# Kernel tuning notes

Hardware: AMD Instinct MI355X
Metric: run time of the kernel (lower is better)

Reference implementation:

```python
import jax, jax.numpy as jnp
import numpy as np

N_NODES = 100000
N_EDGES = 1600000
D = 64          # embedding_dim (in_feats == out_feats)
H = 1           # num_heads
NEG_SLOPE = 0.2


def setup_inputs() -> dict:
    key = jax.random.key(0)
    k = jax.random.split(key, 7)
    feat = jax.random.normal(k[0], (N_NODES, D), dtype=jnp.float32)
    W = jax.random.normal(k[1], (D, H * D), dtype=jnp.float32) * (1.0 / np.sqrt(D))
    attn_l = jax.random.normal(k[2], (1, H, D), dtype=jnp.float32) * (1.0 / np.sqrt(D))
    attn_r = jax.random.normal(k[3], (1, H, D), dtype=jnp.float32) * (1.0 / np.sqrt(D))
    bias = jnp.zeros((H * D,), dtype=jnp.float32)
    src = jax.random.randint(k[4], (N_EDGES,), 0, N_NODES, dtype=jnp.int32)
    dst = jax.random.randint(k[5], (N_EDGES,), 0, N_NODES, dtype=jnp.int32)
    return {"feat": feat, "W": W, "attn_l": attn_l, "attn_r": attn_r,
            "bias": bias, "src": src, "dst": dst}


def reference(feat, W, attn_l, attn_r, bias, src, dst):
    # fc (no bias), view to [N, H, D_out]
    ft = (feat @ W).reshape(-1, H, D)                       # [N, H, D]
    # per-node attention halves
    el = jnp.sum(ft * attn_l, axis=-1, keepdims=True)       # [N, H, 1]
    er = jnp.sum(ft * attn_r, axis=-1, keepdims=True)       # [N, H, 1]
    # edge score: u_add_v then leaky_relu
    e = el[src] + er[dst]                                    # [E, H, 1]
    e = jnp.where(e > 0, e, NEG_SLOPE * e)
    # edge softmax over incoming edges of each destination node
    emax = jax.ops.segment_max(e, dst, num_segments=N_NODES)  # [N, H, 1]
    e_exp = jnp.exp(e - emax[dst])
    denom = jax.ops.segment_sum(e_exp, dst, num_segments=N_NODES)  # [N, H, 1]
    a = e_exp / denom[dst]                                   # [E, H, 1]
    # u_mul_e + sum aggregation to destination
    m = ft[src] * a                                          # [E, H, D]
    rst = jax.ops.segment_sum(m, dst, num_segments=N_NODES)  # [N, H, D]
    # residual (Identity since in_feats == out_feats) + bias
    rst = rst + feat.reshape(-1, H, D)
    rst = rst + bias.reshape(1, H, D)
    return rst
```

## Files before the change

### kernel.cpp

```cpp
#include <hip/hip_runtime.h>
#include <hip/hip_fp16.h>
#include <math.h>

#define NN 100000
#define NE 1600000
#define D 64
#define NEG_SLOPE 0.2f
#define NBKT 391
#define NB1 196
#define CHUNK 8192
#define BSLOT 5120

typedef __attribute__((ext_vector_type(8))) short short8;
typedef __attribute__((ext_vector_type(4))) float f32x4;

template<int CTRL>
__device__ __forceinline__ float dpp_add(float x) {
    int y = __builtin_amdgcn_update_dpp(0, __float_as_int(x), CTRL, 0xf, 0xf, true);
    return x + __int_as_float(y);
}
template<int CTRL>
__device__ __forceinline__ float dpp_max(float x) {
    int xi = __float_as_int(x);
    int y = __builtin_amdgcn_update_dpp(xi, xi, CTRL, 0xf, 0xf, false);
    return fmaxf(x, __int_as_float(y));
}
__device__ __forceinline__ float wave_sum63(float x) {
    x = dpp_add<0x111>(x); x = dpp_add<0x112>(x); x = dpp_add<0x114>(x);
    x = dpp_add<0x118>(x); x = dpp_add<0x142>(x); x = dpp_add<0x143>(x);
    return x;
}
__device__ __forceinline__ float wave_max63(float x) {
    x = dpp_max<0x111>(x); x = dpp_max<0x112>(x); x = dpp_max<0x114>(x);
    x = dpp_max<0x118>(x); x = dpp_max<0x142>(x); x = dpp_max<0x143>(x);
    return x;
}
__device__ __forceinline__ float rdlane_f(float v, int l) {
    return __int_as_float(__builtin_amdgcn_readlane(__float_as_int(v), l));
}
__device__ __forceinline__ unsigned bf16_1(float f) {
    unsigned x = __float_as_uint(f);
    return (x + 0x7fffu + ((x >> 16) & 1u)) >> 16;
}
__device__ __forceinline__ unsigned bfpack(float a, float b) {
    return bf16_1(a) | (bf16_1(b) << 16);
}

__global__ __launch_bounds__(256) void k_bin(const int* __restrict__ src,
                                             const int* __restrict__ dst,
                                             unsigned* __restrict__ bcnt,
                                             unsigned* __restrict__ binned) {
    __shared__ unsigned lh[NBKT];
    int t = threadIdx.x;
    unsigned b0 = blockIdx.x * CHUNK;
    unsigned b1 = min(b0 + CHUNK, (unsigned)NE);
    unsigned n4 = (b1 - b0) >> 2;
    for (int k = t; k < NBKT; k += 256) lh[k] = 0u;
    __syncthreads();
    const int4* d4 = (const int4*)(dst + b0);
    const int4* s4 = (const int4*)(src + b0);
    for (unsigned i = t; i < n4; i += 256) {
        int4 v = d4[i];
        atomicAdd(&lh[((unsigned)v.x) >> 8], 1u);
        atomicAdd(&lh[((unsigned)v.y) >> 8], 1u);
        atomicAdd(&lh[((unsigned)v.z) >> 8], 1u);
        atomicAdd(&lh[((unsigned)v.w) >> 8], 1u);
    }
    __syncthreads();
    for (int k = t; k < NBKT; k += 256) {
        unsigned c = lh[k];
        if (c) lh[k] = (unsigned)k * BSLOT + atomicAdd(&bcnt[k], c);
    }
    __syncthreads();
    for (unsigned i = t; i < n4; i += 256) {
        int4 dv = d4[i];
        int4 sv = s4[i];
        { unsigned d_=(unsigned)dv.x, s_=(unsigned)sv.x;
          unsigned pos=atomicAdd(&lh[d_>>8],1u); binned[pos]=(s_<<8)|(d_&255u); }
        { unsigned d_=(unsigned)dv.y, s_=(unsigned)sv.y;
          unsigned pos=atomicAdd(&lh[d_>>8],1u); binned[pos]=(s_<<8)|(d_&255u); }
        { unsigned d_=(unsigned)dv.z, s_=(unsigned)sv.z;
          unsigned pos=atomicAdd(&lh[d_>>8],1u); binned[pos]=(s_<<8)|(d_&255u); }
        { unsigned d_=(unsigned)dv.w, s_=(unsigned)sv.w;
          unsigned pos=atomicAdd(&lh[d_>>8],1u); binned[pos]=(s_<<8)|(d_&255u); }
    }
}

__global__ __launch_bounds__(256) void k_bsort(const unsigned* __restrict__ bcnt,
                                               const unsigned* __restrict__ binned,
                                               int* __restrict__ perm,
                                               uint2* __restrict__ rowBE) {
    __shared__ unsigned lh[256];
    __shared__ unsigned cur[256];
    __shared__ unsigned stage[BSLOT];
    int t = threadIdx.x;
    int b = blockIdx.x;
    unsigned beg = (unsigned)b * BSLOT;
    unsigned cnt = bcnt[b];
    lh[t] = 0u;
    __syncthreads();
    for (unsigned i = t; i < cnt; i += 256) {
        unsigned w = binned[beg + i];
        stage[i] = w;
        atomicAdd(&lh[w & 255u], 1u);
    }
    __syncthreads();
    for (int off = 1; off < 256; off <<= 1) {
        unsigned u = (t >= off) ? lh[t - off] : 0u;
        __syncthreads();
        lh[t] += u;
        __syncthreads();
    }
    unsigned start = (t == 0) ? 0u : lh[t - 1];
    unsigned node = ((unsigned)b << 8) + (unsigned)t;
    if (node < NN) {
        uint2 be; be.x = beg + start; be.y = beg + lh[t];
        rowBE[node] = be;
    }
    cur[t] = start;
    __syncthreads();
    for (unsigned i = t; i < cnt; i += 256) {
        unsigned w = stage[i];
        unsigned pos = atomicAdd(&cur[w & 255u], 1u);
        perm[beg + pos] = (int)(w >> 8);
    }
}

__global__ __launch_bounds__(256) void k1_mfma(const float* __restrict__ feat,
                                               const float* __restrict__ W,
                                               const float* __restrict__ attn_l,
                                               const float* __restrict__ attn_r,
                                               __half* __restrict__ ft,
                                               float* __restrict__ el,
                                               float* __restrict__ er) {
    __shared__ unsigned short Ab[64 * 64];
    __shared__ unsigned short Bb[64 * 64];
    __shared__ float wlS[64], wrS[64];
    int t = threadIdx.x;
    int n0 = blockIdx.x * 64;

    {
        int k = t >> 2, s = t & 3;
        float pl = 0.f, pr = 0.f;
        #pragma unroll
        for (int q = 0; q < 4; ++q) {
            int seg = s + q * 4;
            float4 f = *(const float4*)(W + k * 64 + seg * 4);
            float4 a = *(const float4*)(attn_l + seg * 4);
            float4 b = *(const float4*)(attn_r + seg * 4);
            pl += f.x*a.x + f.y*a.y + f.z*a.z + f.w*a.w;
            pr += f.x*b.x + f.y*b.y + f.z*b.z + f.w*b.w;
        }
        pl += __shfl_xor(pl, 1, 64); pl += __shfl_xor(pl, 2, 64);
        pr += __shfl_xor(pr, 1, 64); pr += __shfl_xor(pr, 2, 64);
        if (s == 0) { wlS[k] = pl; wrS[k] = pr; }
    }
    {
        int j = t & 63, g = t >> 6;
        unsigned m = (unsigned)((j & 7) << 4);
        #pragma unroll
        for (int i = 0; i < 8; ++i) {
            int k0 = g * 16 + i * 2;
            float w0 = W[k0 * 64 + j];
            float w1 = W[(k0 + 1) * 64 + j];
            *(unsigned*)((char*)Bb + j * 128 + (((unsigned)(k0 * 2)) ^ m)) = bfpack(w0, w1);
        }
    }
    __syncthreads();
    {
        int r = t >> 2, s = t & 3;
        int n = n0 + r;
        bool valid = n < NN;
        const float* fp = feat + (size_t)(valid ? n : (NN - 1)) * D;
        float pl = 0.f, pr = 0.f;
        unsigned m = (unsigned)((r & 7) << 4);
        #pragma unroll
        for (int q = 0; q < 4; ++q) {
            int seg = s + q * 4;
            float4 f = *(const float4*)(fp + seg * 4);
            float4 a = *(const float4*)(wlS + seg * 4);
            float4 b = *(const float4*)(wrS + seg * 4);
            pl += f.x*a.x + f.y*a.y + f.z*a.z + f.w*a.w;
            pr += f.x*b.x + f.y*b.y + f.z*b.z + f.w*b.w;
            uint2 pk;
            pk.x = bfpack(f.x, f.y);
            pk.y = bfpack(f.z, f.w);
            *(uint2*)((char*)Ab + r * 128 + (((unsigned)(seg * 8)) ^ m)) = pk;
        }
        pl += __shfl_xor(pl, 1, 64); pl += __shfl_xor(pl, 2, 64);
        pr += __shfl_xor(pr, 1, 64); pr += __shfl_xor(pr, 2, 64);
        if (s == 0 && valid) { el[n] = pl; er[n] = pr; }
    }
    __syncthreads();

    int w = t >> 6, l = t & 63;
    int lr = l & 15, lg = l >> 4;
    f32x4 acc0 = {0.f,0.f,0.f,0.f};
    f32x4 acc1 = {0.f,0.f,0.f,0.f};
    f32x4 acc2 = {0.f,0.f,0.f,0.f};
    f32x4 acc3 = {0.f,0.f,0.f,0.f};

    int jrow = w * 16 + lr;
    unsigned bm = (unsigned)((jrow & 7) << 4);
    short8 bf0 = *(const short8*)((char*)Bb + jrow * 128 + (((unsigned)(0 + lg * 16)) ^ bm));
    short8 bf1 = *(const short8*)((char*)Bb + jrow * 128 + (((unsigned)(64 + lg * 16)) ^ bm));

    #pragma unroll
    for (int rt = 0; rt < 4; ++rt) {
        int arow = rt * 16 + lr;
        unsigned am = (unsigned)((arow & 7) << 4);
        short8 a0 = *(const short8*)((char*)Ab + arow * 128 + (((unsigned)(0 + lg * 16)) ^ am));
        short8 a1 = *(const short8*)((char*)Ab + arow * 128 + (((unsigned)(64 + lg * 16)) ^ am));
        f32x4 acc = (rt == 0) ? acc0 : (rt == 1) ? acc1 : (rt == 2) ? acc2 : acc3;
        acc = __builtin_amdgcn_mfma_f32_16x16x32_bf16(a0, bf0, acc, 0, 0, 0);
        acc = __builtin_amdgcn_mfma_f32_16x16x32_bf16(a1, bf1, acc, 0, 0, 0);
        if (rt == 0) acc0 = acc; else if (rt == 1) acc1 = acc;
        else if (rt == 2) acc2 = acc; else acc3 = acc;
    }

    int col = w * 16 + lr;
    #pragma unroll
    for (int rt = 0; rt < 4; ++rt) {
        f32x4 acc = (rt == 0) ? acc0 : (rt == 1) ? acc1 : (rt == 2) ? acc2 : acc3;
        #pragma unroll
        for (int i = 0; i < 4; ++i) {
            int row = rt * 16 + lg * 4 + i;
            int nn = n0 + row;
            if (nn < NN) ft[(size_t)nn * D + col] = __float2half(acc[i]);
        }
    }
}

__device__ __noinline__ void agg_node64(int d, int lane, unsigned beg, unsigned end,
                                        const int* __restrict__ perm_src,
                                        const float* __restrict__ el, float er_d,
                                        const __half* __restrict__ ft,
                                        const float* __restrict__ feat,
                                        const float* __restrict__ bias,
                                        float* __restrict__ out) {
    float acc = 0.0f;
    float s = 0.0f;
    float m = -INFINITY;
    for (unsigned base = beg; base < end; base += 64) {
        unsigned i = base + lane;
        float e = -INFINITY;
        if (i < end) {
            int sid2 = perm_src[i];
            float v = el[sid2] + er_d;
            e = v > 0.0f ? v : NEG_SLOPE * v;
        }
        m = fmaxf(m, rdlane_f(wave_max63(e), 63));
    }
    for (unsigned base = beg; base < end; base += 64) {
        unsigned i = base + lane;
        float exx = 0.0f;
        if (i < end) {
            int sid2 = perm_src[i];
            float v = el[sid2] + er_d;
            v = v > 0.0f ? v : NEG_SLOPE * v;
            exx = __expf(v - m);
        }
        s += rdlane_f(wave_sum63(exx), 63);
    }
    for (unsigned jj = beg; jj < end; ++jj) {
        int sj = perm_src[jj];
        float v = el[sj] + er_d;
        v = v > 0.0f ? v : NEG_SLOPE * v;
        acc = fmaf(__half2float(ft[((size_t)sj << 6) + lane]), __expf(v - m), acc);
    }
    acc /= s;
    out[(size_t)d * D + lane] = acc + feat[(size_t)d * D + lane] + bias[lane];
}

#define LOAD8(B, J) do { \
    const __half* _p0 = (const __half*)(ftb + (((unsigned)__builtin_amdgcn_readlane(sid, (J) + 0)) << 7)); \
    const __half* _p1 = (const __half*)(ftb + (((unsigned)__builtin_amdgcn_readlane(sid, (J) + 1)) << 7)); \
    const __half* _p2 = (const __half*)(ftb + (((unsigned)__builtin_amdgcn_readlane(sid, (J) + 2)) << 7)); \
    const __half* _p3 = (const __half*)(ftb + (((unsigned)__builtin_amdgcn_readlane(sid, (J) + 3)) << 7)); \
    const __half* _p4 = (const __half*)(ftb + (((unsigned)__builtin_amdgcn_readlane(sid, (J) + 4)) << 7)); \
    const __half* _p5 = (const __half*)(ftb + (((unsigned)__builtin_amdgcn_readlane(sid, (J) + 5)) << 7)); \
    const __half* _p6 = (const __half*)(ftb + (((unsigned)__builtin_amdgcn_readlane(sid, (J) + 6)) << 7)); \
    const __half* _p7 = (const __half*)(ftb + (((unsigned)__builtin_amdgcn_readlane(sid, (J) + 7)) << 7)); \
    B##0 = _p0[lane]; B##1 = _p1[lane]; B##2 = _p2[lane]; B##3 = _p3[lane]; \
    B##4 = _p4[lane]; B##5 = _p5[lane]; B##6 = _p6[lane]; B##7 = _p7[lane]; \
} while (0)

#define FMA8(B, J) do { \
    acc = fmaf(__half2float(B##0), rdlane_f(ex, (J) + 0), acc); \
    acc = fmaf(__half2float(B##1), rdlane_f(ex, (J) + 1), acc); \
    acc = fmaf(__half2float(B##2), rdlane_f(ex, (J) + 2), acc); \
    acc = fmaf(__half2float(B##3), rdlane_f(ex, (J) + 3), acc); \
    acc = fmaf(__half2float(B##4), rdlane_f(ex, (J) + 4), acc); \
    acc = fmaf(__half2float(B##5), rdlane_f(ex, (J) + 5), acc); \
    acc = fmaf(__half2float(B##6), rdlane_f(ex, (J) + 6), acc); \
    acc = fmaf(__half2float(B##7), rdlane_f(ex, (J) + 7), acc); \
} while (0)

__global__ __launch_bounds__(256) void k_agg(const uint2* __restrict__ rowBE,
                                             const int* __restrict__ perm_src,
                                             const float* __restrict__ el,
                                             const float* __restrict__ er,
                                             const __half* __restrict__ ft,
                                             const float* __restrict__ feat,
                                             const float* __restrict__ bias,
                                             float* __restrict__ out) {
    int gid = blockIdx.x * 256 + threadIdx.x;
    int d = gid >> 6;
    int lane = gid & 63;
    if (d >= NN) return;

    uint2 be = rowBE[d];
    unsigned beg = be.x;
    int deg = (int)(be.y - be.x);
    float er_d = er[d];

    if (deg > 64) {
        agg_node64(d, lane, be.x, be.y, perm_src, el, er_d, ft, feat, bias, out);
        return;
    }
    if (deg == 0) {
        out[(size_t)d * D + lane] = feat[(size_t)d * D + lane] + bias[lane];
        return;
    }

    int sid = perm_src[beg + ((lane < deg) ? lane : 0)];
    float elv = el[sid];

    const char* ftb = (const char*)ft;

    __half c0, c1, c2, c3, c4, c5, c6, c7;
    __half n0, n1, n2, n3, n4, n5, n6, n7;
    LOAD8(c, 0);

    float e = elv + er_d;
    e = e > 0.0f ? e : NEG_SLOPE * e;
    float ex = (lane < deg) ? __expf(e) : 0.0f;
    float s = rdlane_f(wave_sum63(ex), 63);
    float inv_s = __frcp_rn(s);

    float acc = 0.0f;
    int j = 0;
    while (true) {
        bool more = (j + 8) < deg;
        if (more) LOAD8(n, j + 8);
        FMA8(c, j);
        j += 8;
        if (!more) break;
        bool more2 = (j + 8) < deg;
        if (more2) LOAD8(c, j + 8);
        FMA8(n, j);
        j += 8;
        if (!more2) break;
    }
    acc *= inv_s;
    out[(size_t)d * D + lane] = acc + feat[(size_t)d * D + lane] + bias[lane];
}

extern "C" void kernel_launch(void* const* d_in, const int* in_sizes, int n_in,
                              void* d_out, int out_size, void* d_ws, size_t ws_size,
                              hipStream_t stream) {
    const float* feat   = (const float*)d_in[0];
    const float* W      = (const float*)d_in[1];
    const float* attn_l = (const float*)d_in[2];
    const float* attn_r = (const float*)d_in[3];
    const float* bias   = (const float*)d_in[4];
    const int*   src    = (const int*)d_in[5];
    const int*   dst    = (const int*)d_in[6];
    float* out = (float*)d_out;

    char* ws = (char*)d_ws;
    __half*   ft     = (__half*)(ws);
    unsigned* binned = (unsigned*)(ws);
    float*    el     = (float*)(ws + 12800000);
    float*    er     = (float*)(ws + 13200000);
    int*      perm   = (int*)(ws + 13600000);
    uint2*    rowBE  = (uint2*)(ws + 21607680);
    unsigned* bcnt   = (unsigned*)(ws + 22407680);

    hipMemsetAsync(bcnt, 0, NBKT * sizeof(unsigned), stream);
    k_bin<<<NB1, 256, 0, stream>>>(src, dst, bcnt, binned);
    k_bsort<<<NBKT, 256, 0, stream>>>(bcnt, binned, perm, rowBE);
    k1_mfma<<<(NN + 63) / 64, 256, 0, stream>>>(feat, W, attn_l, attn_r, ft, el, er);
    k_agg<<<(NN * 64 + 255) / 256, 256, 0, stream>>>(rowBE, perm, el, er,
                                                     ft, feat, bias, out);
}
```

Measured before the change: 101.7 us.

## Merge edge binning and MFMA projection into one heterogeneous launch

Combines the edge-binning kernel and the feature projection GEMM into a single launch, with block index ranges choosing which role each block plays, so the two independent phases run concurrently and one launch boundary goes away. Because binned previously aliased the ft buffer, binned moves to its own workspace region so both can be live at once. The gather in aggregation now forms a byte offset by OR-ing in the lane index instead of indexing through a pointer. The cost is more workspace, and shared memory is sized for the larger of the two roles, which can limit occupancy for the binning blocks.

```diff
diff --git a/kernel.cpp b/kernel.cpp
--- a/kernel.cpp
+++ b/kernel.cpp
@@ -10,6 +10,7 @@
 #define NB1 196
 #define CHUNK 8192
 #define BSLOT 5120
+#define NTILE 1563
 
 typedef __attribute__((ext_vector_type(8))) short short8;
 typedef __attribute__((ext_vector_type(4))) float f32x4;
@@ -46,98 +47,58 @@
     return bf16_1(a) | (bf16_1(b) << 16);
 }
 
-__global__ __launch_bounds__(256) void k_bin(const int* __restrict__ src,
-                                             const int* __restrict__ dst,
-                                             unsigned* __restrict__ bcnt,
-                                             unsigned* __restrict__ binned) {
-    __shared__ unsigned lh[NBKT];
+__global__ __launch_bounds__(256) void k_pre(
+    const int* __restrict__ src, const int* __restrict__ dst,
+    const float* __restrict__ feat, const float* __restrict__ W,
+    const float* __restrict__ attn_l, const float* __restrict__ attn_r,
+    unsigned* __restrict__ bcnt, unsigned* __restrict__ binned,
+    __half* __restrict__ ft, float* __restrict__ el, float* __restrict__ er)
+{
+    __shared__ __align__(16) char smem[16896];
     int t = threadIdx.x;
-    unsigned b0 = blockIdx.x * CHUNK;
-    unsigned b1 = min(b0 + CHUNK, (unsigned)NE);
-    unsigned n4 = (b1 - b0) >> 2;
-    for (int k = t; k < NBKT; k += 256) lh[k] = 0u;
-    __syncthreads();
-    const int4* d4 = (const int4*)(dst + b0);
-    const int4* s4 = (const int4*)(src + b0);
-    for (unsigned i = t; i < n4; i += 256) {
-        int4 v = d4[i];
-        atomicAdd(&lh[((unsigned)v.x) >> 8], 1u);
-        atomicAdd(&lh[((unsigned)v.y) >> 8], 1u);
-        atomicAdd(&lh[((unsigned)v.z) >> 8], 1u);
-        atomicAdd(&lh[((unsigned)v.w) >> 8], 1u);
-    }
-    __syncthreads();
-    for (int k = t; k < NBKT; k += 256) {
-        unsigned c = lh[k];
-        if (c) lh[k] = (unsigned)k * BSLOT + atomicAdd(&bcnt[k], c);
-    }
-    __syncthreads();
-    for (unsigned i = t; i < n4; i += 256) {
-        int4 dv = d4[i];
-        int4 sv = s4[i];
-        { unsigned d_=(unsigned)dv.x, s_=(unsigned)sv.x;
-          unsigned pos=atomicAdd(&lh[d_>>8],1u); binned[pos]=(s_<<8)|(d_&255u); }
-        { unsigned d_=(unsigned)dv.y, s_=(unsigned)sv.y;
-          unsigned pos=atomicAdd(&lh[d_>>8],1u); binned[pos]=(s_<<8)|(d_&255u); }
-        { unsigned d_=(unsigned)dv.z, s_=(unsigned)sv.z;
-          unsigned pos=atomicAdd(&lh[d_>>8],1u); binned[pos]=(s_<<8)|(d_&255u); }
-        { unsigned d_=(unsigned)dv.w, s_=(unsigned)sv.w;
-          unsigned pos=atomicAdd(&lh[d_>>8],1u); binned[pos]=(s_<<8)|(d_&255u); }
-    }
-}
-
-__global__ __launch_bounds__(256) void k_bsort(const unsigned* __restrict__ bcnt,
-                                               const unsigned* __restrict__ binned,
-                                               int* __restrict__ perm,
-                                               uint2* __restrict__ rowBE) {
-    __shared__ unsigned lh[256];
-    __shared__ unsigned cur[256];
-    __shared__ unsigned stage[BSLOT];
-    int t = threadIdx.x;
-    int b = blockIdx.x;
-    unsigned beg = (unsigned)b * BSLOT;
-    unsigned cnt = bcnt[b];
-    lh[t] = 0u;
-    __syncthreads();
-    for (unsigned i = t; i < cnt; i += 256) {
-        unsigned w = binned[beg + i];
-        stage[i] = w;
-        atomicAdd(&lh[w & 255u], 1u);
-    }
-    __syncthreads();
-    for (int off = 1; off < 256; off <<= 1) {
-        unsigned u = (t >= off) ? lh[t - off] : 0u;
-        __syncthreads();
-        lh[t] += u;
-        __syncthreads();
-    }
-    unsigned start = (t == 0) ? 0u : lh[t - 1];
-    unsigned node = ((unsigned)b << 8) + (unsigned)t;
-    if (node < NN) {
-        uint2 be; be.x = beg + start; be.y = beg + lh[t];
-        rowBE[node] = be;
-    }
-    cur[t] = start;
-    __syncthreads();
-    for (unsigned i = t; i < cnt; i += 256) {
-        unsigned w = stage[i];
-        unsigned pos = atomicAdd(&cur[w & 255u], 1u);
-        perm[beg + pos] = (int)(w >> 8);
-    }
-}
-
-__global__ __launch_bounds__(256) void k1_mfma(const float* __restrict__ feat,
-                                               const float* __restrict__ W,
-                                               const float* __restrict__ attn_l,
-                                               const float* __restrict__ attn_r,
-                                               __half* __restrict__ ft,
-                                               float* __restrict__ el,
-                                               float* __restrict__ er) {
-    __shared__ unsigned short Ab[64 * 64];
-    __shared__ unsigned short Bb[64 * 64];
-    __shared__ float wlS[64], wrS[64];
-    int t = threadIdx.x;
-    int n0 = blockIdx.x * 64;
+
+    if (blockIdx.x < NB1) {
+        unsigned* lh = (unsigned*)smem;
+        unsigned b0 = blockIdx.x * CHUNK;
+        unsigned b1 = min(b0 + CHUNK, (unsigned)NE);
+        unsigned n4 = (b1 - b0) >> 2;
+        for (int k = t; k < NBKT; k += 256) lh[k] = 0u;
+        __syncthreads();
+        const int4* d4 = (const int4*)(dst + b0);
+        const int4* s4 = (const int4*)(src + b0);
+        for (unsigned i = t; i < n4; i += 256) {
+            int4 v = d4[i];
+            atomicAdd(&lh[((unsigned)v.x) >> 8], 1u);
+            atomicAdd(&lh[((unsigned)v.y) >> 8], 1u);
+            atomicAdd(&lh[((unsigned)v.z) >> 8], 1u);
+            atomicAdd(&lh[((unsigned)v.w) >> 8], 1u);
+        }
+        __syncthreads();
+        for (int k = t; k < NBKT; k += 256) {
+            unsigned c = lh[k];
+            if (c) lh[k] = (unsigned)k * BSLOT + atomicAdd(&bcnt[k], c);
+        }
+        __syncthreads();
+        for (unsigned i = t; i < n4; i += 256) {
+            int4 dv = d4[i];
+            int4 sv = s4[i];
+            { unsigned d_=(unsigned)dv.x, s_=(unsigned)sv.x;
+              unsigned pos=atomicAdd(&lh[d_>>8],1u); binned[pos]=(s_<<8)|(d_&255u); }
+            { unsigned d_=(unsigned)dv.y, s_=(unsigned)sv.y;
+              unsigned pos=atomicAdd(&lh[d_>>8],1u); binned[pos]=(s_<<8)|(d_&255u); }
+            { unsigned d_=(unsigned)dv.z, s_=(unsigned)sv.z;
+              unsigned pos=atomicAdd(&lh[d_>>8],1u); binned[pos]=(s_<<8)|(d_&255u); }
+            { unsigned d_=(unsigned)dv.w, s_=(unsigned)sv.w;
+              unsigned pos=atomicAdd(&lh[d_>>8],1u); binned[pos]=(s_<<8)|(d_&255u); }
+        }
+        return;
+    }
+
+    unsigned short* Ab = (unsigned short*)smem;
+    unsigned short* Bb = (unsigned short*)(smem + 8192);
+    float* wlS = (float*)(smem + 16384);
+    float* wrS = (float*)(smem + 16640);
+    int n0 = (int)(blockIdx.x - NB1) * 64;
 
     {
         int k = t >> 2, s = t & 3;
@@ -231,6 +192,46 @@
     }
 }
 
+__global__ __launch_bounds__(256) void k_bsort(const unsigned* __restrict__ bcnt,
+                                               const unsigned* __restrict__ binned,
+                                               int* __restrict__ perm,
+                                               uint2* __restrict__ rowBE) {
+    __shared__ unsigned lh[256];
+    __shared__ unsigned cur[256];
+    __shared__ unsigned stage[BSLOT];
+    int t = threadIdx.x;
+    int b = blockIdx.x;
+    unsigned beg = (unsigned)b * BSLOT;
+    unsigned cnt = bcnt[b];
+    lh[t] = 0u;
+    __syncthreads();
+    for (unsigned i = t; i < cnt; i += 256) {
+        unsigned w = binned[beg + i];
+        stage[i] = w;
+        atomicAdd(&lh[w & 255u], 1u);
+    }
+    __syncthreads();
+    for (int off = 1; off < 256; off <<= 1) {
+        unsigned u = (t >= off) ? lh[t - off] : 0u;
+        __syncthreads();
+        lh[t] += u;
+        __syncthreads();
+    }
+    unsigned start = (t == 0) ? 0u : lh[t - 1];
+    unsigned node = ((unsigned)b << 8) + (unsigned)t;
+    if (node < NN) {
+        uint2 be; be.x = beg + start; be.y = beg + lh[t];
+        rowBE[node] = be;
+    }
+    cur[t] = start;
+    __syncthreads();
+    for (unsigned i = t; i < cnt; i += 256) {
+        unsigned w = stage[i];
+        unsigned pos = atomicAdd(&cur[w & 255u], 1u);
+        perm[beg + pos] = (int)(w >> 8);
+    }
+}
+
 __device__ __noinline__ void agg_node64(int d, int lane, unsigned beg, unsigned end,
                                         const int* __restrict__ perm_src,
                                         const float* __restrict__ el, float er_d,
@@ -273,16 +274,22 @@
 }
 
 #define LOAD8(B, J) do { \
-    const __half* _p0 = (const __half*)(ftb + (((unsigned)__builtin_amdgcn_readlane(sid, (J) + 0)) << 7)); \
-    const __half* _p1 = (const __half*)(ftb + (((unsigned)__builtin_amdgcn_readlane(sid, (J) + 1)) << 7)); \
-    const __half* _p2 = (const __half*)(ftb + (((unsigned)__builtin_amdgcn_readlane(sid, (J) + 2)) << 7)); \
-    const __half* _p3 = (const __half*)(ftb + (((unsigned)__builtin_amdgcn_readlane(sid, (J) + 3)) << 7)); \
-    const __half* _p4 = (const __half*)(ftb + (((unsigned)__builtin_amdgcn_readlane(sid, (J) + 4)) << 7)); \
-    const __half* _p5 = (const __half*)(ftb + (((unsigned)__builtin_amdgcn_readlane(sid, (J) + 5)) << 7)); \
-    const __half* _p6 = (const __half*)(ftb + (((unsigned)__builtin_amdgcn_readlane(sid, (J) + 6)) << 7)); \
-    const __half* _p7 = (const __half*)(ftb + (((unsigned)__builtin_amdgcn_readlane(sid, (J) + 7)) << 7)); \
-    B##0 = _p0[lane]; B##1 = _p1[lane]; B##2 = _p2[lane]; B##3 = _p3[lane]; \
-    B##4 = _p4[lane]; B##5 = _p5[lane]; B##6 = _p6[lane]; B##7 = _p7[lane]; \
+    unsigned _o0 = (((unsigned)__builtin_amdgcn_readlane(sid, (J) + 0)) << 7) | lb; \
+    unsigned _o1 = (((unsigned)__builtin_amdgcn_readlane(sid, (J) + 1)) << 7) | lb; \
+    unsigned _o2 = (((unsigned)__builtin_amdgcn_readlane(sid, (J) + 2)) << 7) | lb; \
+    unsigned _o3 = (((unsigned)__builtin_amdgcn_readlane(sid, (J) + 3)) << 7) | lb; \
+    unsigned _o4 = (((unsigned)__builtin_amdgcn_readlane(sid, (J) + 4)) << 7) | lb; \
+    unsigned _o5 = (((unsigned)__builtin_amdgcn_readlane(sid, (J) + 5)) << 7) | lb; \
+    unsigned _o6 = (((unsigned)__builtin_amdgcn_readlane(sid, (J) + 6)) << 7) | lb; \
+    unsigned _o7 = (((unsigned)__builtin_amdgcn_readlane(sid, (J) + 7)) << 7) | lb; \
+    B##0 = *(const __half*)(ftb + _o0); \
+    B##1 = *(const __half*)(ftb + _o1); \
+    B##2 = *(const __half*)(ftb + _o2); \
+    B##3 = *(const __half*)(ftb + _o3); \
+    B##4 = *(const __half*)(ftb + _o4); \
+    B##5 = *(const __half*)(ftb + _o5); \
+    B##6 = *(const __half*)(ftb + _o6); \
+    B##7 = *(const __half*)(ftb + _o7); \
 } while (0)
 
 #define FMA8(B, J) do { \
@@ -327,6 +334,7 @@
     float elv = el[sid];
 
     const char* ftb = (const char*)ft;
+    unsigned lb = (unsigned)lane << 1;
 
     __half c0, c1, c2, c3, c4, c5, c6, c7;
     __half n0, n1, n2, n3, n4, n5, n6, n7;
@@ -370,17 +378,17 @@
 
     char* ws = (char*)d_ws;
     __half*   ft     = (__half*)(ws);
-    unsigned* binned = (unsigned*)(ws);
     float*    el     = (float*)(ws + 12800000);
     float*    er     = (float*)(ws + 13200000);
     int*      perm   = (int*)(ws + 13600000);
     uint2*    rowBE  = (uint2*)(ws + 21607680);
     unsigned* bcnt   = (unsigned*)(ws + 22407680);
+    unsigned* binned = (unsigned*)(ws + 22409248);
 
     hipMemsetAsync(bcnt, 0, NBKT * sizeof(unsigned), stream);
-    k_bin<<<NB1, 256, 0, stream>>>(src, dst, bcnt, binned);
+    k_pre<<<NB1 + NTILE, 256, 0, stream>>>(src, dst, feat, W, attn_l, attn_r,
+                                           bcnt, binned, ft, el, er);
     k_bsort<<<NBKT, 256, 0, stream>>>(bcnt, binned, perm, rowBE);
-    k1_mfma<<<(NN + 63) / 64, 256, 0, stream>>>(feat, W, attn_l, attn_r, ft, el, er);
     k_agg<<<(NN * 64 + 255) / 256, 256, 0, stream>>>(rowBE, perm, el, er,
                                                      ft, feat, bias, out);
 }
```

Result: faster. 93.58 us (-8.0%).
